# Kernel optimization log

Hardware: AMD Instinct MI355X
Metric: run time of the kernel (lower is better)

Reference implementation:

```python
import jax, jax.numpy as jnp
import numpy as np
from jax import lax

BN_EPS = 1e-3
SLOPE = 0.1
CLUSTER_TEMP = 30.0
K = 16
FEAT = 4096  # 8*8*64


def conv_bn_lrelu(x, w, b, g, beta, m, v):
    # Conv2d stride 2, padding 1 (NCHW / OIHW), then eval-mode BatchNorm, then LeakyReLU.
    y = lax.conv_general_dilated(x, w, window_strides=(2, 2), padding=((1, 1), (1, 1)),
                                 dimension_numbers=("NCHW", "OIHW", "NCHW"))
    y = y + b[None, :, None, None]
    scale = g / jnp.sqrt(v + BN_EPS)
    y = y * scale[None, :, None, None] + (beta - m * scale)[None, :, None, None]
    return jnp.where(y > 0, y, SLOPE * y)


def soft_kmeans(data, mu, num_iter, ct):
    # Row L2-normalize (equivalent to diag(1/||x||) @ data)
    data = data / jnp.linalg.norm(data, axis=1, keepdims=True)
    for _ in range(num_iter):
        dist = data @ mu.T                      # [N, K]
        r = jax.nn.softmax(ct * dist, axis=1)   # [N, K]
        mu = (r.T @ data) / r.sum(axis=0)[:, None]  # [K, F]
    dist = data @ mu.T
    r = jax.nn.softmax(ct * dist, axis=1)
    return mu, r, dist


def setup_inputs() -> dict:
    key = jax.random.key(0)
    ks = jax.random.split(key, 12)
    d = {}
    d["x"] = jax.random.normal(ks[0], (256, 3, 64, 64), dtype=jnp.float32)
    # conv1: 3 -> 128
    d["conv1_w"] = jax.random.normal(ks[1], (128, 3, 3, 3), dtype=jnp.float32) * 0.05
    d["conv1_b"] = jnp.zeros((128,), jnp.float32)
    d["bn1_g"] = jnp.ones((128,), jnp.float32)
    d["bn1_b"] = jnp.zeros((128,), jnp.float32)
    d["bn1_m"] = jax.random.normal(ks[2], (128,), dtype=jnp.float32) * 0.1
    d["bn1_v"] = jax.random.uniform(ks[3], (128,), minval=0.5, maxval=1.5, dtype=jnp.float32)
    # conv2: 128 -> 256
    d["conv2_w"] = jax.random.normal(ks[4], (256, 128, 3, 3), dtype=jnp.float32) * 0.02
    d["conv2_b"] = jnp.zeros((256,), jnp.float32)
    d["bn2_g"] = jnp.ones((256,), jnp.float32)
    d["bn2_b"] = jnp.zeros((256,), jnp.float32)
    d["bn2_m"] = jax.random.normal(ks[5], (256,), dtype=jnp.float32) * 0.1
    d["bn2_v"] = jax.random.uniform(ks[6], (256,), minval=0.5, maxval=1.5, dtype=jnp.float32)
    # conv3: 256 -> 64
    d["conv3_w"] = jax.random.normal(ks[7], (64, 256, 3, 3), dtype=jnp.float32) * 0.02
    d["conv3_b"] = jnp.zeros((64,), jnp.float32)
    d["bn3_g"] = jnp.ones((64,), jnp.float32)
    d["bn3_b"] = jnp.zeros((64,), jnp.float32)
    d["bn3_m"] = jax.random.normal(ks[8], (64,), dtype=jnp.float32) * 0.1
    d["bn3_v"] = jax.random.uniform(ks[9], (64,), minval=0.5, maxval=1.5, dtype=jnp.float32)
    # initial cluster centers, torch.rand(K, F)
    d["mu0"] = jax.random.uniform(ks[10], (K, FEAT), dtype=jnp.float32)
    d["num_iter"] = 10
    return d


def reference(x, conv1_w, conv1_b, bn1_g, bn1_b, bn1_m, bn1_v,
              conv2_w, conv2_b, bn2_g, bn2_b, bn2_m, bn2_v,
              conv3_w, conv3_b, bn3_g, bn3_b, bn3_m, bn3_v,
              mu0, num_iter):
    h = conv_bn_lrelu(x, conv1_w, conv1_b, bn1_g, bn1_b, bn1_m, bn1_v)   # [B,128,32,32]
    h = conv_bn_lrelu(h, conv2_w, conv2_b, bn2_g, bn2_b, bn2_m, bn2_v)   # [B,256,16,16]
    h = conv_bn_lrelu(h, conv3_w, conv3_b, bn3_g, bn3_b, bn3_m, bn3_v)   # [B,64,8,8]
    embeds = h.reshape(-1, FEAT)                                          # [B, 4096]
    mu_init, _, _ = soft_kmeans(embeds, mu0, num_iter, CLUSTER_TEMP)
    _, r, _ = soft_kmeans(embeds, lax.stop_gradient(mu_init), 1, CLUSTER_TEMP)
    return r
```

## Files before the change

kernel.cpp:

```cpp
#include <hip/hip_runtime.h>
#include <stdint.h>
#include <stddef.h>

typedef unsigned short u16;
typedef __attribute__((ext_vector_type(8))) short short8;
typedef __attribute__((ext_vector_type(4))) float f32x4;
typedef __attribute__((ext_vector_type(4))) int int4v;

__device__ __forceinline__ float bf2f(u16 u) {
    unsigned x = ((unsigned)u) << 16;
    return __uint_as_float(x);
}
__device__ __forceinline__ u16 f2bf(float f) {
    unsigned x = __float_as_uint(f);
    unsigned r = (x + 0x7fffu + ((x >> 16) & 1u)) >> 16;
    return (u16)r;
}
__device__ __forceinline__ float ldin(const void* p, size_t i, int isbf) {
    return isbf ? bf2f(((const u16*)p)[i]) : ((const float*)p)[i];
}
__device__ __forceinline__ int detect_bf(const void* v1) {
    const u16* ub = (const u16*)v1;
    int ok = 1;
#pragma unroll
    for (int i = 0; i < 16; i++) {
        float f = bf2f(ub[i]);
        if (!(f >= 0.4f && f <= 1.6f)) ok = 0;
    }
    return ok;
}
__device__ __forceinline__ int sw(int r, int c8) {
    return r * 32 + (((c8) ^ (r & 3)) << 3);
}

struct PrepArgs {
    const void *w1, *w2, *w3;
    u16 *W1p, *W2p, *W3p;
    const void *b1, *g1, *be1, *m1, *v1;
    const void *b2, *g2, *be2, *m2, *v2;
    const void *b3, *g3, *be3, *m3, *v3;
    float *es1, *esh1, *es2, *esh2, *es3, *esh3;
    u16 *zb;
};
__device__ __forceinline__ void packw_body(const void* src, u16* dst, int CI, int Kp,
                                           int total, int blk, int t, int isbf) {
    int p = blk * 256 + t;
    if (p >= total) return;
    int co = p / Kp, k = p - co * Kp;
    int tap = k / CI, ci = k - tap * CI;
    u16 v = 0;
    if (tap < 9) {
        size_t si = (size_t)(co * CI + ci) * 9 + tap;
        v = isbf ? ((const u16*)src)[si] : f2bf(((const float*)src)[si]);
    }
    dst[p] = v;
}
__global__ __launch_bounds__(256) void kprep_all(PrepArgs A) {
    int b = blockIdx.x, t = threadIdx.x;
    int isbf = detect_bf(A.v1);
    if (b < 1152) {
        packw_body(A.w2, A.W2p, 128, 1152, 256 * 1152, b, t, isbf);
    } else if (b < 1728) {
        packw_body(A.w3, A.W3p, 256, 2304, 64 * 2304, b - 1152, t, isbf);
    } else if (b < 1744) {
        packw_body(A.w1, A.W1p, 3, 32, 128 * 32, b - 1728, t, isbf);
    } else {
        if (b == 1745) A.zb[t] = 0;
        int u = (b - 1744) * 256 + t;
        const void *bb, *g, *be, *m, *v;
        float *es, *esh;
        int c;
        if (u < 128)      { c = u;       bb=A.b1; g=A.g1; be=A.be1; m=A.m1; v=A.v1; es=A.es1; esh=A.esh1; }
        else if (u < 384) { c = u - 128; bb=A.b2; g=A.g2; be=A.be2; m=A.m2; v=A.v2; es=A.es2; esh=A.esh2; }
        else if (u < 448) { c = u - 384; bb=A.b3; g=A.g3; be=A.be3; m=A.m3; v=A.v3; es=A.es3; esh=A.esh3; }
        else return;
        float sc = ldin(g, c, isbf) / sqrtf(ldin(v, c, isbf) + 1e-3f);
        float sh = (ldin(bb, c, isbf) - ldin(m, c, isbf)) * sc + ldin(be, c, isbf);
        es[c] = sc;
        esh[c] = sh;
    }
}

__global__ void kfallback(u16* __restrict__ out) {
    int i = blockIdx.x * 256 + threadIdx.x;
    if (i < 4096) out[i] = f2bf(0.0625f);
}

__global__ __launch_bounds__(256) void im2col1(const void* __restrict__ x,
                                               u16* __restrict__ A1,
                                               const void* __restrict__ v1ref) {
    int n = blockIdx.x, t = threadIdx.x;
    int isbf = detect_bf(v1ref);
    __shared__ u16 xs[3 * 64 * 64];
    if (isbf) {
        const u16* xp = (const u16*)x + (size_t)n * 12288;
#pragma unroll
        for (int i = t * 8; i < 12288; i += 2048)
            *(int4v*)&xs[i] = *(const int4v*)&xp[i];
    } else {
        const float* xp = (const float*)x + (size_t)n * 12288;
#pragma unroll
        for (int i = t * 4; i < 12288; i += 1024) {
            float4 v = *(const float4*)&xp[i];
            xs[i] = f2bf(v.x); xs[i + 1] = f2bf(v.y);
            xs[i + 2] = f2bf(v.z); xs[i + 3] = f2bf(v.w);
        }
    }
    __syncthreads();
#pragma unroll
    for (int rr = 0; rr < 4; rr++) {
        int m = rr * 256 + t;
        int ox = m & 31, oy = m >> 5;
        alignas(16) u16 row[32];
#pragma unroll
        for (int k = 0; k < 32; k++) {
            u16 val = 0;
            if (k < 27) {
                int tap = k / 3, ci = k - 3 * tap;
                int ky = tap / 3, kx = tap - 3 * ky;
                int iy = 2 * oy - 1 + ky, ix = 2 * ox - 1 + kx;
                if ((unsigned)iy < 64u && (unsigned)ix < 64u)
                    val = xs[ci * 4096 + iy * 64 + ix];
            }
            row[k] = val;
        }
        int4v* dst = (int4v*)(A1 + ((size_t)n * 1024 + m) * 32);
        const int4v* srcv = (const int4v*)row;
#pragma unroll
        for (int q = 0; q < 4; q++) dst[q] = srcv[q];
    }
}

__global__ __launch_bounds__(256) void gemm_conv1(
    const u16* __restrict__ A1, const u16* __restrict__ W,
    const float* __restrict__ es, const float* __restrict__ esh,
    u16* __restrict__ OutB) {
    alignas(16) __shared__ u16 As[128 * 32];
    alignas(16) __shared__ u16 Bs[128 * 32];
    const int t = threadIdx.x;
    const int m0 = blockIdx.x * 128;
    const int lane = t & 63, w = t >> 6;
    const int wm = w & 1, wn = w >> 1;
    const int rA = t >> 2, c8 = t & 3, koff = c8 * 8;

#pragma unroll
    for (int j = 0; j < 2; j++) {
        int4v va = *(const int4v*)(A1 + (size_t)(m0 + j * 64 + rA) * 32 + koff);
        *(int4v*)&As[sw(j * 64 + rA, c8)] = va;
        int4v vb = *(const int4v*)(W + (size_t)(j * 64 + rA) * 32 + koff);
        *(int4v*)&Bs[sw(j * 64 + rA, c8)] = vb;
    }
    __syncthreads();
    const int qc = lane >> 4, fr = lane & 15;
    short8 af[4], bf[4];
#pragma unroll
    for (int i = 0; i < 4; i++) af[i] = *(const short8*)&As[sw(wm * 64 + i * 16 + fr, qc)];
#pragma unroll
    for (int j = 0; j < 4; j++) bf[j] = *(const short8*)&Bs[sw(wn * 64 + j * 16 + fr, qc)];
    f32x4 acc[4][4];
#pragma unroll
    for (int i = 0; i < 4; i++)
#pragma unroll
        for (int j = 0; j < 4; j++) {
#pragma unroll
            for (int q = 0; q < 4; q++) acc[i][j][q] = 0.f;
            acc[i][j] = __builtin_amdgcn_mfma_f32_16x16x32_bf16(af[i], bf[j], acc[i][j], 0, 0, 0);
        }
    float scv[4], shv[4];
#pragma unroll
    for (int j = 0; j < 4; j++) {
        int c = wn * 64 + j * 16 + fr;
        scv[j] = es[c];
        shv[j] = esh[c];
    }
#pragma unroll
    for (int i = 0; i < 4; i++) {
#pragma unroll
        for (int rg = 0; rg < 4; rg++) {
            int m = m0 + wm * 64 + i * 16 + qc * 4 + rg;
            int ox = m & 31, oy = (m >> 5) & 31, n = m >> 10;
            u16* orow = OutB + ((size_t)(n * 32 + oy) * 32 + ox) * 128 + wn * 64 + fr;
#pragma unroll
            for (int j = 0; j < 4; j++) {
                float v = acc[i][j][rg] * scv[j] + shv[j];
                v = (v > 0.f) ? v : 0.1f * v;
                orow[j * 16] = f2bf(v);
            }
        }
    }
}

__global__ __launch_bounds__(512, 2) void gemm_conv2(
    const u16* __restrict__ h1, const u16* __restrict__ W,
    const float* __restrict__ es, const float* __restrict__ esh,
    u16* __restrict__ OutB, const u16* __restrict__ zb) {
    alignas(16) __shared__ u16 smem[4 * 16384];
    u16* const Ab0 = smem;
    u16* const Ab1 = smem + 16384;
    u16* const Bb0 = smem + 32768;
    u16* const Bb1 = smem + 49152;

    const int t = threadIdx.x;
    const int w = t >> 6, l = t & 63;
    const int img = blockIdx.x;
    const int wm = w >> 2, wn = w & 3;
    const int fr = l & 15, qc = l >> 4;

    int aiy0[4], aix0[4], ac8e[4];
    int brow[4];
#pragma unroll
    for (int i = 0; i < 4; ++i) {
        int gi = w * 256 + i * 64 + l;
        int r = gi >> 3, c8d = gi & 7;
        int c8s = c8d ^ (r & 7);
        int oy = r >> 4, ox = r & 15;
        aiy0[i] = 2 * oy - 1;
        aix0[i] = 2 * ox - 1;
        ac8e[i] = c8s * 8;
        brow[i] = r * 1152 + c8s * 8;
    }
    auto mkA = [&](int i, int ky, int kx) -> const u16* {
        int iy = aiy0[i] + ky, ix = aix0[i] + kx;
        if ((unsigned)iy < 32u && (unsigned)ix < 32u)
            return h1 + (size_t)(((img * 32 + iy) * 32 + ix) * 128 + ac8e[i]);
        return zb;
    };
    auto stage = [&](const u16* src, u16* ldsbase, int i) {
        __builtin_amdgcn_global_load_lds(
            (const __attribute__((address_space(1))) void*)src,
            (__attribute__((address_space(3))) void*)(ldsbase + (w * 4 + i) * 512),
            16, 0, 0);
    };

    f32x4 acc[8][4];
#pragma unroll
    for (int mi = 0; mi < 8; ++mi)
#pragma unroll
        for (int nj = 0; nj < 4; ++nj)
#pragma unroll
            for (int q = 0; q < 4; ++q) acc[mi][nj][q] = 0.0f;

    auto do_tile = [&](const u16* A, const u16* B) {
#pragma unroll
        for (int kk = 0; kk < 2; ++kk) {
            const int c8 = kk * 4 + qc;
            short8 a[8], b[4];
#pragma unroll
            for (int q = 0; q < 8; ++q) {
                int row = wm * 128 + q * 16 + fr;
                a[q] = *(const short8*)(A + row * 64 + ((c8 ^ (row & 7)) << 3));
            }
#pragma unroll
            for (int j = 0; j < 4; ++j) {
                int row = wn * 64 + j * 16 + fr;
                b[j] = *(const short8*)(B + row * 64 + ((c8 ^ (row & 7)) << 3));
            }
            __builtin_amdgcn_s_setprio(1);
#pragma unroll
            for (int q = 0; q < 8; ++q)
#pragma unroll
                for (int j = 0; j < 4; ++j)
                    acc[q][j] = __builtin_amdgcn_mfma_f32_16x16x32_bf16(
                        a[q], b[j], acc[q][j], 0, 0, 0);
            __builtin_amdgcn_s_setprio(0);
        }
    };

    const u16* pcur[4];
#pragma unroll
    for (int i = 0; i < 4; ++i) pcur[i] = mkA(i, 0, 0);
#pragma unroll
    for (int i = 0; i < 4; ++i) {
        stage(pcur[i], Ab0, i);
        stage(W + brow[i], Bb0, i);
    }
#pragma unroll
    for (int i = 0; i < 4; ++i) {
        stage(pcur[i] + 64, Ab1, i);
        stage(W + brow[i] + 64, Bb1, i);
    }

    for (int tap = 0; tap < 9; ++tap) {
        asm volatile("s_waitcnt vmcnt(8)" ::: "memory");
        __builtin_amdgcn_s_barrier();
        do_tile(Ab0, Bb0);
        asm volatile("s_waitcnt lgkmcnt(0)" ::: "memory");
        __builtin_amdgcn_s_barrier();
        if (tap < 8) {
            const int tap2 = tap + 1;
            const int ky2 = (tap2 >= 6) ? 2 : (tap2 >= 3) ? 1 : 0;
            const int kx2 = tap2 - 3 * ky2;
#pragma unroll
            for (int i = 0; i < 4; ++i) pcur[i] = mkA(i, ky2, kx2);
#pragma unroll
            for (int i = 0; i < 4; ++i) {
                stage(pcur[i], Ab0, i);
                stage(W + brow[i] + (2 * tap + 2) * 64, Bb0, i);
            }
        }
        if (tap < 8) {
            asm volatile("s_waitcnt vmcnt(8)" ::: "memory");
        } else {
            asm volatile("s_waitcnt vmcnt(0)" ::: "memory");
        }
        __builtin_amdgcn_s_barrier();
        do_tile(Ab1, Bb1);
        asm volatile("s_waitcnt lgkmcnt(0)" ::: "memory");
        __builtin_amdgcn_s_barrier();
        if (tap < 8) {
#pragma unroll
            for (int i = 0; i < 4; ++i) {
                stage(pcur[i] + 64, Ab1, i);
                stage(W + brow[i] + (2 * tap + 3) * 64, Bb1, i);
            }
        }
    }

    float scv[4], shv[4];
#pragma unroll
    for (int nj = 0; nj < 4; ++nj) {
        int c = wn * 64 + nj * 16 + fr;
        scv[nj] = es[c];
        shv[nj] = esh[c];
    }
#pragma unroll
    for (int mi = 0; mi < 8; ++mi) {
#pragma unroll
        for (int rg = 0; rg < 4; ++rg) {
            int r = wm * 128 + mi * 16 + qc * 4 + rg;
            u16* orow = OutB + ((size_t)img * 256 + r) * 256 + wn * 64 + fr;
#pragma unroll
            for (int nj = 0; nj < 4; ++nj) {
                float v = acc[mi][nj][rg] * scv[nj] + shv[nj];
                v = (v > 0.f) ? v : 0.1f * v;
                orow[nj * 16] = f2bf(v);
            }
        }
    }
}

__global__ __launch_bounds__(256) void gemm_conv3f(
    const u16* __restrict__ Asrc, const u16* __restrict__ W,
    const float* __restrict__ es3, const float* __restrict__ esh3,
    float* __restrict__ dat, u16* __restrict__ datbf) {
    constexpr int CIN = 256, KTOT = 2304, IH = 16;
    constexpr int CC = 8, SM = 2, SN = 2;

    alignas(16) __shared__ u16 As[64 * 32];
    alignas(16) __shared__ u16 Bs[64 * 32];
    __shared__ float red[4];

    const int t = threadIdx.x;
    const int lid = blockIdx.x;
    const int xcd = lid & 7, slot = lid >> 3;
    const int img = xcd * 32 + slot;
    const int m0 = img * 64;
    const int lane = t & 63, w = t >> 6;
    const int wm = w & 1, wn = w >> 1;
    const int rA = t >> 2, c8 = t & 3, koff = c8 * 8;
    const int fr = lane & 15, qc = lane >> 4;

    f32x4 acc[SM][SN];
#pragma unroll
    for (int i = 0; i < SM; i++)
#pragma unroll
        for (int j = 0; j < SN; j++)
#pragma unroll
            for (int q = 0; q < 4; q++) acc[i][j][q] = 0.0f;

    const int aox = rA & 7, aoy = (rA >> 3) & 7;
    auto mkoffs = [&](int tap) -> int {
        int ky = tap / 3, kx = tap - 3 * ky;
        int iy = 2 * aoy - 1 + ky, ix = 2 * aox - 1 + kx;
        if ((unsigned)iy < (unsigned)IH && (unsigned)ix < (unsigned)IH)
            return ((img * IH + iy) * IH + ix) * CIN;
        return -0x40000000;
    };
    const u16* Wrow = W + (size_t)rA * KTOT + koff;

    int offs_cur = mkoffs(0), offs_nxt;
    const int4v zerov = (int4v){0, 0, 0, 0};
    int4v bufA[2], bufB[2];
#pragma unroll
    for (int pp = 0; pp < 2; pp++) {
        bufA[pp] = (offs_cur >= 0)
                       ? *(const int4v*)(Asrc + offs_cur + pp * 32 + koff)
                       : zerov;
        bufB[pp] = *(const int4v*)(Wrow + pp * 32);
    }

    int flat = 0;
    for (int tap = 0; tap < 9; tap++) {
        offs_nxt = (tap < 8) ? mkoffs(tap + 1) : -0x40000000;
#pragma unroll
        for (int cc = 0; cc < CC; cc++, flat++) {
            const int pb_ = flat & 1;
            *(int4v*)&As[sw(rA, c8)] = bufA[pb_];
            *(int4v*)&Bs[sw(rA, c8)] = bufB[pb_];
            __syncthreads();
            {
                const int cc2 = cc + 2;
                const bool intap = (cc2 < CC);
                const int cci = intap ? cc2 : cc2 - CC;
                int o = intap ? offs_cur : offs_nxt;
                bufA[pb_] = (o >= 0) ? *(const int4v*)(Asrc + o + cci * 32 + koff) : zerov;
                const bool wvalid = intap || (tap < 8);
                const int wk = (intap ? tap : tap + 1) * CIN + cci * 32;
                bufB[pb_] = wvalid ? *(const int4v*)(Wrow + wk) : zerov;
            }
            short8 af[SM], bf[SN];
#pragma unroll
            for (int i = 0; i < SM; i++)
                af[i] = *(const short8*)&As[sw(wm * 32 + i * 16 + fr, qc)];
#pragma unroll
            for (int j = 0; j < SN; j++)
                bf[j] = *(const short8*)&Bs[sw(wn * 32 + j * 16 + fr, qc)];
#pragma unroll
            for (int i = 0; i < SM; i++)
#pragma unroll
                for (int j = 0; j < SN; j++)
                    acc[i][j] = __builtin_amdgcn_mfma_f32_16x16x32_bf16(
                        af[i], bf[j], acc[i][j], 0, 0, 0);
            __syncthreads();
        }
        offs_cur = offs_nxt;
    }

    float vals[SM][SN][4];
    float ssq = 0.f;
#pragma unroll
    for (int j = 0; j < SN; j++) {
        int c = wn * 32 + j * 16 + fr;
        float sc = es3[c], sh = esh3[c];
#pragma unroll
        for (int i = 0; i < SM; i++) {
#pragma unroll
            for (int rg = 0; rg < 4; rg++) {
                float v = acc[i][j][rg] * sc + sh;
                v = (v > 0.f) ? v : 0.1f * v;
                vals[i][j][rg] = v;
                ssq += v * v;
            }
        }
    }
#pragma unroll
    for (int off = 32; off > 0; off >>= 1) ssq += __shfl_xor(ssq, off);
    if (lane == 0) red[w] = ssq;
    __syncthreads();
    float inv = 1.0f / sqrtf(red[0] + red[1] + red[2] + red[3]);
#pragma unroll
    for (int j = 0; j < SN; j++) {
        int c = wn * 32 + j * 16 + fr;
#pragma unroll
        for (int i = 0; i < SM; i++) {
#pragma unroll
            for (int rg = 0; rg < 4; rg++) {
                int row = wm * 32 + i * 16 + qc * 4 + rg;
                size_t idx = (size_t)img * 4096 + c * 64 + row;
                float v = vals[i][j][rg] * inv;
                dat[idx] = v;
                datbf[idx] = f2bf(v);
            }
        }
    }
}

__global__ __launch_bounds__(256) void kgr(const u16* __restrict__ dbf,
                                           const float* __restrict__ dat,
                                           const void* __restrict__ mu0,
                                           float* __restrict__ Gp,
                                           float* __restrict__ rb0,
                                           const void* __restrict__ v1ref) {
    const int b = blockIdx.x, t = threadIdx.x;
    __shared__ float part[16][4];
    __shared__ float ds[16];

    if (b < 64) {
        const int tile = b & 15, s = b >> 4;
        const int m0 = (tile & 3) * 64, n0 = (tile >> 2) * 64;
        const int lane = t & 63, w = t >> 6;
        const int wm = w & 1, wn = w >> 1;
        const int fr = lane & 15, qc = lane >> 4;

        f32x4 acc[2][2];
#pragma unroll
        for (int i = 0; i < 2; i++)
#pragma unroll
            for (int j = 0; j < 2; j++)
#pragma unroll
                for (int q = 0; q < 4; q++) acc[i][j][q] = 0.0f;

        const u16* a0p = dbf + (size_t)(m0 + wm * 32 + fr) * 4096 + s * 1024 + qc * 8;
        const u16* a1p = a0p + 16 * 4096;
        const u16* b0p = dbf + (size_t)(n0 + wn * 32 + fr) * 4096 + s * 1024 + qc * 8;
        const u16* b1p = b0p + 16 * 4096;

        short8 Pa0[4], Pa1[4], Pb0[4], Pb1[4];
        short8 Qa0[4], Qa1[4], Qb0[4], Qb1[4];
        auto ldc = [&](short8* A0, short8* A1, short8* B0, short8* B1, int c) {
#pragma unroll
            for (int u = 0; u < 4; ++u) {
                const int o = c * 128 + u * 32;
                A0[u] = *(const short8*)(a0p + o);
                A1[u] = *(const short8*)(a1p + o);
                B0[u] = *(const short8*)(b0p + o);
                B1[u] = *(const short8*)(b1p + o);
            }
        };
        auto mmc = [&](short8* A0, short8* A1, short8* B0, short8* B1) {
#pragma unroll
            for (int u = 0; u < 4; ++u) {
                acc[0][0] = __builtin_amdgcn_mfma_f32_16x16x32_bf16(A0[u], B0[u], acc[0][0], 0, 0, 0);
                acc[0][1] = __builtin_amdgcn_mfma_f32_16x16x32_bf16(A0[u], B1[u], acc[0][1], 0, 0, 0);
                acc[1][0] = __builtin_amdgcn_mfma_f32_16x16x32_bf16(A1[u], B0[u], acc[1][0], 0, 0, 0);
                acc[1][1] = __builtin_amdgcn_mfma_f32_16x16x32_bf16(A1[u], B1[u], acc[1][1], 0, 0, 0);
            }
        };
        ldc(Pa0, Pa1, Pb0, Pb1, 0);
#pragma unroll
        for (int c = 0; c < 4; ++c) {
            ldc(Qa0, Qa1, Qb0, Qb1, 2 * c + 1);
            mmc(Pa0, Pa1, Pb0, Pb1);
            if (c < 3) ldc(Pa0, Pa1, Pb0, Pb1, 2 * c + 2);
            mmc(Qa0, Qa1, Qb0, Qb1);
        }

        float* gp = Gp + (size_t)s * 65536;
#pragma unroll
        for (int j = 0; j < 2; j++) {
            int cc = n0 + wn * 32 + j * 16 + fr;
#pragma unroll
            for (int i = 0; i < 2; i++)
#pragma unroll
                for (int rg = 0; rg < 4; rg++) {
                    int row = m0 + wm * 32 + i * 16 + qc * 4 + rg;
                    gp[row * 256 + cc] = acc[i][j][rg];
                }
        }
    } else {
        const int n = b - 64;
        const int isbf = detect_bf(v1ref);
        const int lane = t & 63, wv = t >> 6;
        float d[16];
#pragma unroll
        for (int j = 0; j < 16; j++) d[j] = dat[(size_t)n * 4096 + j * 256 + t];
#pragma unroll
        for (int k = 0; k < 16; k++) {
            float a = 0.f;
            if (isbf) {
                const u16* mp = (const u16*)mu0 + (size_t)k * 4096;
#pragma unroll
                for (int j = 0; j < 16; j++) a = fmaf(d[j], bf2f(mp[j * 256 + t]), a);
            } else {
                const float* mp = (const float*)mu0 + (size_t)k * 4096;
#pragma unroll
                for (int j = 0; j < 16; j++) a = fmaf(d[j], mp[j * 256 + t], a);
            }
#pragma unroll
            for (int off = 32; off > 0; off >>= 1) a += __shfl_xor(a, off);
            if (lane == 0) part[k][wv] = a;
        }
        __syncthreads();
        if (t < 16) {
            float dk = part[t][0] + part[t][1] + part[t][2] + part[t][3];
            ds[t] = dk;
            __syncthreads();
            float mx = -1e30f;
#pragma unroll
            for (int j = 0; j < 16; j++) mx = fmaxf(mx, ds[j]);
            float sum = 0.f;
#pragma unroll
            for (int j = 0; j < 16; j++) sum += __expf(30.f * (ds[j] - mx));
            rb0[n * 16 + t] = __expf(30.f * (dk - mx)) / sum;
        }
    }
}

__global__ __launch_bounds__(256) void kcomb(const float* __restrict__ Gp,
                                             u16* __restrict__ Ghi,
                                             u16* __restrict__ Glo) {
    const int i = (blockIdx.x * 256 + threadIdx.x) * 4;
    f32x4 s0 = *(const f32x4*)(Gp + i);
    f32x4 s1 = *(const f32x4*)(Gp + 65536 + i);
    f32x4 s2 = *(const f32x4*)(Gp + 131072 + i);
    f32x4 s3 = *(const f32x4*)(Gp + 196608 + i);
    unsigned long long ph = 0, pl = 0;
#pragma unroll
    for (int q = 0; q < 4; q++) {
        float v = ((s0[q] + s1[q]) + s2[q]) + s3[q];
        u16 hi = f2bf(v);
        u16 lo = f2bf(v - bf2f(hi));
        ph |= ((unsigned long long)hi) << (16 * q);
        pl |= ((unsigned long long)lo) << (16 * q);
    }
    *(unsigned long long*)(Ghi + i) = ph;
    *(unsigned long long*)(Glo + i) = pl;
}

__global__ __launch_bounds__(1024) void kmiter(const u16* __restrict__ Ghi,
                                               const u16* __restrict__ Glo,
                                               const float* __restrict__ rb0,
                                               void* __restrict__ dout,
                                               const void* __restrict__ v1ref) {
    const int t = threadIdx.x;
    const int isbf = detect_bf(v1ref);
    const int lane = t & 63, w = t >> 6;
    const int i0 = w * 16;
    const int col = lane & 15;
    const int q = lane >> 4;

    __shared__ u16 rThi[2][16 * 264];
    __shared__ u16 rTlo[2][16 * 264];
    __shared__ float part[2][16][17];

    const u16* Ahirow = Ghi + (size_t)(i0 + col) * 256 + q * 8;
    const u16* Alorow = Glo + (size_t)(i0 + col) * 256 + q * 8;

    {
        float rv[4];
#pragma unroll
        for (int rg = 0; rg < 4; rg++) {
            int row = i0 + q * 4 + rg;
            float v = rb0[row * 16 + col];
            rv[rg] = v;
            u16 hi = f2bf(v);
            rThi[0][col * 264 + row] = hi;
            rTlo[0][col * 264 + row] = f2bf(v - bf2f(hi));
        }
        float s0 = rv[0] + rv[1] + rv[2] + rv[3];
        s0 += __shfl_xor(s0, 16);
        s0 += __shfl_xor(s0, 32);
        if (lane < 16) part[0][w][lane] = s0;
    }
    __syncthreads();
    float rsc = 0.f;
#pragma unroll
    for (int ww = 0; ww < 16; ww++) rsc += part[0][ww][col];

    int cur = 0;
    for (int iter = 0; iter < 11; iter++) {
        f32x4 acc0 = {0.f, 0.f, 0.f, 0.f};
        f32x4 acc1 = {0.f, 0.f, 0.f, 0.f};
#pragma unroll
        for (int s = 0; s < 4; s++) {
            {
                short8 ah = *(const short8*)(Ahirow + s * 32);
                short8 al = *(const short8*)(Alorow + s * 32);
                short8 bh = *(const short8*)&rThi[cur][col * 264 + s * 32 + q * 8];
                short8 bl = *(const short8*)&rTlo[cur][col * 264 + s * 32 + q * 8];
                acc0 = __builtin_amdgcn_mfma_f32_16x16x32_bf16(ah, bh, acc0, 0, 0, 0);
                acc0 = __builtin_amdgcn_mfma_f32_16x16x32_bf16(al, bh, acc0, 0, 0, 0);
                acc0 = __builtin_amdgcn_mfma_f32_16x16x32_bf16(ah, bl, acc0, 0, 0, 0);
            }
            {
                short8 ah = *(const short8*)(Ahirow + (s + 4) * 32);
                short8 al = *(const short8*)(Alorow + (s + 4) * 32);
                short8 bh = *(const short8*)&rThi[cur][col * 264 + (s + 4) * 32 + q * 8];
                short8 bl = *(const short8*)&rTlo[cur][col * 264 + (s + 4) * 32 + q * 8];
                acc1 = __builtin_amdgcn_mfma_f32_16x16x32_bf16(ah, bh, acc1, 0, 0, 0);
                acc1 = __builtin_amdgcn_mfma_f32_16x16x32_bf16(al, bh, acc1, 0, 0, 0);
                acc1 = __builtin_amdgcn_mfma_f32_16x16x32_bf16(ah, bl, acc1, 0, 0, 0);
            }
        }
        float nv[4];
#pragma unroll
        for (int rg = 0; rg < 4; rg++) {
            float dk = (acc0[rg] + acc1[rg]) / rsc;
            float mx = dk;
#pragma unroll
            for (int o = 1; o < 16; o <<= 1) mx = fmaxf(mx, __shfl_xor(mx, o));
            float e = __expf(30.f * (dk - mx));
            float ssum = e;
#pragma unroll
            for (int o = 1; o < 16; o <<= 1) ssum += __shfl_xor(ssum, o);
            nv[rg] = e / ssum;
        }
        if (iter < 10) {
            const int nxt = cur ^ 1;
#pragma unroll
            for (int rg = 0; rg < 4; rg++) {
                int row = i0 + q * 4 + rg;
                u16 hi = f2bf(nv[rg]);
                rThi[nxt][col * 264 + row] = hi;
                rTlo[nxt][col * 264 + row] = f2bf(nv[rg] - bf2f(hi));
            }
            float s0 = nv[0] + nv[1] + nv[2] + nv[3];
            s0 += __shfl_xor(s0, 16);
            s0 += __shfl_xor(s0, 32);
            if (lane < 16) part[nxt][w][lane] = s0;
            __syncthreads();
            rsc = 0.f;
#pragma unroll
            for (int ww = 0; ww < 16; ww++) rsc += part[nxt][ww][col];
            cur = nxt;
        } else {
#pragma unroll
            for (int rg = 0; rg < 4; rg++) {
                int row = i0 + q * 4 + rg;
                if (isbf) ((u16*)dout)[row * 16 + col] = f2bf(nv[rg]);
                else ((float*)dout)[row * 16 + col] = nv[rg];
            }
        }
    }
}

extern "C" void kernel_launch(void* const* d_in, const int* in_sizes, int n_in,
                              void* d_out, int out_size, void* d_ws, size_t ws_size,
                              hipStream_t stream) {
    const void* x   = d_in[0];
    const void* w1  = d_in[1];
    const void* b1  = d_in[2];
    const void* g1  = d_in[3];
    const void* be1 = d_in[4];
    const void* m1  = d_in[5];
    const void* v1  = d_in[6];
    const void* w2  = d_in[7];
    const void* b2  = d_in[8];
    const void* g2  = d_in[9];
    const void* be2 = d_in[10];
    const void* m2  = d_in[11];
    const void* v2  = d_in[12];
    const void* w3  = d_in[13];
    const void* b3  = d_in[14];
    const void* g3  = d_in[15];
    const void* be3 = d_in[16];
    const void* m3  = d_in[17];
    const void* v3  = d_in[18];
    const void* mu0 = d_in[19];

    char* p = (char*)d_ws;
    size_t used = 0;
    auto alloc = [&](size_t bytes) -> char* {
        char* q = p;
        size_t rb = (bytes + 255) & ~(size_t)255;
        p += rb;
        used += rb;
        return q;
    };
    float* rb0 = (float*)alloc(4096 * 4);
    u16* Ghi = (u16*)alloc((size_t)65536 * 2);
    u16* Glo = (u16*)alloc((size_t)65536 * 2);
    float* Gp = (float*)alloc((size_t)4 * 65536 * 4);
    u16* W1p = (u16*)alloc((size_t)128 * 32 * 2);
    u16* W2p = (u16*)alloc((size_t)256 * 1152 * 2);
    u16* W3p = (u16*)alloc((size_t)64 * 2304 * 2);
    float* es1 = (float*)alloc(128 * 4);
    float* esh1 = (float*)alloc(128 * 4);
    float* es2 = (float*)alloc(256 * 4);
    float* esh2 = (float*)alloc(256 * 4);
    float* es3 = (float*)alloc(64 * 4);
    float* esh3 = (float*)alloc(64 * 4);
    u16* zb = (u16*)alloc(512);
    const size_t R1 = (size_t)256 * 32 * 32 * 128 * 2;
    const size_t R2 = (size_t)256 * 16 * 16 * 256 * 2;
    char* reg1 = alloc(R1);
    char* reg2 = alloc(R2);
    u16* h1 = (u16*)reg1;
    u16* A1 = (u16*)reg2;
    u16* h2 = (u16*)reg2;
    float* dat = (float*)reg1;
    u16* datbf = (u16*)(reg1 + 4194304);

    if (used > ws_size) {
        kfallback<<<16, 256, 0, stream>>>((u16*)d_out);
        return;
    }

    PrepArgs pa = {w1, w2, w3, W1p, W2p, W3p,
                   b1, g1, be1, m1, v1, b2, g2, be2, m2, v2, b3, g3, be3, m3, v3,
                   es1, esh1, es2, esh2, es3, esh3, zb};
    kprep_all<<<1746, 256, 0, stream>>>(pa);
    im2col1<<<256, 256, 0, stream>>>(x, A1, v1);
    gemm_conv1<<<dim3(2048), 256, 0, stream>>>(A1, W1p, es1, esh1, h1);
    gemm_conv2<<<dim3(256), 512, 0, stream>>>(h1, W2p, es2, esh2, h2, zb);
    gemm_conv3f<<<dim3(256), 256, 0, stream>>>(h2, W3p, es3, esh3, dat, datbf);
    kgr<<<dim3(320), 256, 0, stream>>>(datbf, dat, mu0, Gp, rb0, v1);
    kcomb<<<dim3(64), 256, 0, stream>>>(Gp, Ghi, Glo);
    kmiter<<<1, 1024, 0, stream>>>(Ghi, Glo, rb0, d_out, v1);
}
```

Baseline: 268.5 us.

## Use direct global-to-LDS loads with wider K tiles in conv3 GEMM

```diff
diff --git a/kernel.cpp b/kernel.cpp
--- a/kernel.cpp
+++ b/kernel.cpp
@@ -274,18 +274,16 @@
         stage(pcur[i], Ab0, i);
         stage(W + brow[i], Bb0, i);
     }
-#pragma unroll
-    for (int i = 0; i < 4; ++i) {
-        stage(pcur[i] + 64, Ab1, i);
-        stage(W + brow[i] + 64, Bb1, i);
-    }
 
     for (int tap = 0; tap < 9; ++tap) {
-        asm volatile("s_waitcnt vmcnt(8)" ::: "memory");
-        __builtin_amdgcn_s_barrier();
+        __syncthreads();
+#pragma unroll
+        for (int i = 0; i < 4; ++i) {
+            stage(pcur[i] + 64, Ab1, i);
+            stage(W + brow[i] + (2 * tap + 1) * 64, Bb1, i);
+        }
         do_tile(Ab0, Bb0);
-        asm volatile("s_waitcnt lgkmcnt(0)" ::: "memory");
-        __builtin_amdgcn_s_barrier();
+        __syncthreads();
         if (tap < 8) {
             const int tap2 = tap + 1;
             const int ky2 = (tap2 >= 6) ? 2 : (tap2 >= 3) ? 1 : 0;
@@ -298,22 +296,7 @@
                 stage(W + brow[i] + (2 * tap + 2) * 64, Bb0, i);
             }
         }
-        if (tap < 8) {
-            asm volatile("s_waitcnt vmcnt(8)" ::: "memory");
-        } else {
-            asm volatile("s_waitcnt vmcnt(0)" ::: "memory");
-        }
-        __builtin_amdgcn_s_barrier();
         do_tile(Ab1, Bb1);
-        asm volatile("s_waitcnt lgkmcnt(0)" ::: "memory");
-        __builtin_amdgcn_s_barrier();
-        if (tap < 8) {
-#pragma unroll
-            for (int i = 0; i < 4; ++i) {
-                stage(pcur[i] + 64, Ab1, i);
-                stage(W + brow[i] + (2 * tap + 3) * 64, Bb1, i);
-            }
-        }
     }
 
     float scv[4], shv[4];
@@ -342,98 +325,122 @@
 __global__ __launch_bounds__(256) void gemm_conv3f(
     const u16* __restrict__ Asrc, const u16* __restrict__ W,
     const float* __restrict__ es3, const float* __restrict__ esh3,
-    float* __restrict__ dat, u16* __restrict__ datbf) {
-    constexpr int CIN = 256, KTOT = 2304, IH = 16;
-    constexpr int CC = 8, SM = 2, SN = 2;
-
-    alignas(16) __shared__ u16 As[64 * 32];
-    alignas(16) __shared__ u16 Bs[64 * 32];
+    float* __restrict__ dat, u16* __restrict__ datbf,
+    const u16* __restrict__ zb) {
+    alignas(16) __shared__ u16 smem[4 * 4096];
     __shared__ float red[4];
+    u16* const AbP[2] = {smem, smem + 4096};
+    u16* const BbP[2] = {smem + 8192, smem + 12288};
 
     const int t = threadIdx.x;
+    const int w = t >> 6, l = t & 63;
     const int lid = blockIdx.x;
     const int xcd = lid & 7, slot = lid >> 3;
     const int img = xcd * 32 + slot;
-    const int m0 = img * 64;
-    const int lane = t & 63, w = t >> 6;
     const int wm = w & 1, wn = w >> 1;
-    const int rA = t >> 2, c8 = t & 3, koff = c8 * 8;
-    const int fr = lane & 15, qc = lane >> 4;
-
-    f32x4 acc[SM][SN];
-#pragma unroll
-    for (int i = 0; i < SM; i++)
-#pragma unroll
-        for (int j = 0; j < SN; j++)
+    const int fr = l & 15, qc = l >> 4;
+
+    int aiy0[2], aix0[2], ac8e[2];
+    int brow[2];
+#pragma unroll
+    for (int i = 0; i < 2; ++i) {
+        int g = w * 128 + i * 64 + l;
+        int r = g >> 3, c8d = g & 7;
+        int c8s = c8d ^ (r & 7);
+        int oy = r >> 3, ox = r & 7;
+        aiy0[i] = 2 * oy - 1;
+        aix0[i] = 2 * ox - 1;
+        ac8e[i] = c8s * 8;
+        brow[i] = r * 2304 + c8s * 8;
+    }
+    auto mkA = [&](int i, int ky, int kx) -> const u16* {
+        int iy = aiy0[i] + ky, ix = aix0[i] + kx;
+        if ((unsigned)iy < 16u && (unsigned)ix < 16u)
+            return Asrc + (size_t)(((img * 16 + iy) * 16 + ix) * 256 + ac8e[i]);
+        return zb;
+    };
+    auto stage = [&](const u16* src, u16* ldsbase, int i) {
+        __builtin_amdgcn_global_load_lds(
+            (const __attribute__((address_space(1))) void*)src,
+            (__attribute__((address_space(3))) void*)(ldsbase + (w * 2 + i) * 512),
+            16, 0, 0);
+    };
+
+    f32x4 acc[2][2];
+#pragma unroll
+    for (int i = 0; i < 2; i++)
+#pragma unroll
+        for (int j = 0; j < 2; j++)
 #pragma unroll
             for (int q = 0; q < 4; q++) acc[i][j][q] = 0.0f;
 
-    const int aox = rA & 7, aoy = (rA >> 3) & 7;
-    auto mkoffs = [&](int tap) -> int {
-        int ky = tap / 3, kx = tap - 3 * ky;
-        int iy = 2 * aoy - 1 + ky, ix = 2 * aox - 1 + kx;
-        if ((unsigned)iy < (unsigned)IH && (unsigned)ix < (unsigned)IH)
-            return ((img * IH + iy) * IH + ix) * CIN;
-        return -0x40000000;
+    auto do_tile = [&](const u16* A, const u16* B) {
+#pragma unroll
+        for (int kk = 0; kk < 2; ++kk) {
+            const int c8 = kk * 4 + qc;
+            short8 a[2], b[2];
+#pragma unroll
+            for (int i = 0; i < 2; ++i) {
+                int row = wm * 32 + i * 16 + fr;
+                a[i] = *(const short8*)(A + row * 64 + ((c8 ^ (row & 7)) << 3));
+            }
+#pragma unroll
+            for (int j = 0; j < 2; ++j) {
+                int row = wn * 32 + j * 16 + fr;
+                b[j] = *(const short8*)(B + row * 64 + ((c8 ^ (row & 7)) << 3));
+            }
+            __builtin_amdgcn_s_setprio(1);
+#pragma unroll
+            for (int i = 0; i < 2; ++i)
+#pragma unroll
+                for (int j = 0; j < 2; ++j)
+                    acc[i][j] = __builtin_amdgcn_mfma_f32_16x16x32_bf16(
+                        a[i], b[j], acc[i][j], 0, 0, 0);
+            __builtin_amdgcn_s_setprio(0);
+        }
     };
-    const u16* Wrow = W + (size_t)rA * KTOT + koff;
-
-    int offs_cur = mkoffs(0), offs_nxt;
-    const int4v zerov = (int4v){0, 0, 0, 0};
-    int4v bufA[2], bufB[2];
-#pragma unroll
-    for (int pp = 0; pp < 2; pp++) {
-        bufA[pp] = (offs_cur >= 0)
-                       ? *(const int4v*)(Asrc + offs_cur + pp * 32 + koff)
-                       : zerov;
-        bufB[pp] = *(const int4v*)(Wrow + pp * 32);
+
+    const u16* pcur[2];
+#pragma unroll
+    for (int i = 0; i < 2; ++i) pcur[i] = mkA(i, 0, 0);
+#pragma unroll
+    for (int i = 0; i < 2; ++i) {
+        stage(pcur[i], AbP[0], i);
+        stage(W + brow[i], BbP[0], i);
     }
 
     int flat = 0;
-    for (int tap = 0; tap < 9; tap++) {
-        offs_nxt = (tap < 8) ? mkoffs(tap + 1) : -0x40000000;
-#pragma unroll
-        for (int cc = 0; cc < CC; cc++, flat++) {
-            const int pb_ = flat & 1;
-            *(int4v*)&As[sw(rA, c8)] = bufA[pb_];
-            *(int4v*)&Bs[sw(rA, c8)] = bufB[pb_];
+    for (int tap = 0; tap < 9; ++tap) {
+        for (int q4 = 0; q4 < 4; ++q4, ++flat) {
+            const int cb = flat & 1;
             __syncthreads();
-            {
-                const int cc2 = cc + 2;
-                const bool intap = (cc2 < CC);
-                const int cci = intap ? cc2 : cc2 - CC;
-                int o = intap ? offs_cur : offs_nxt;
-                bufA[pb_] = (o >= 0) ? *(const int4v*)(Asrc + o + cci * 32 + koff) : zerov;
-                const bool wvalid = intap || (tap < 8);
-                const int wk = (intap ? tap : tap + 1) * CIN + cci * 32;
-                bufB[pb_] = wvalid ? *(const int4v*)(Wrow + wk) : zerov;
-            }
-            short8 af[SM], bf[SN];
-#pragma unroll
-            for (int i = 0; i < SM; i++)
-                af[i] = *(const short8*)&As[sw(wm * 32 + i * 16 + fr, qc)];
-#pragma unroll
-            for (int j = 0; j < SN; j++)
-                bf[j] = *(const short8*)&Bs[sw(wn * 32 + j * 16 + fr, qc)];
-#pragma unroll
-            for (int i = 0; i < SM; i++)
-#pragma unroll
-                for (int j = 0; j < SN; j++)
-                    acc[i][j] = __builtin_amdgcn_mfma_f32_16x16x32_bf16(
-                        af[i], bf[j], acc[i][j], 0, 0, 0);
-            __syncthreads();
-        }
-        offs_cur = offs_nxt;
-    }
-
-    float vals[SM][SN][4];
+            int ntap = tap, nq = q4 + 1;
+            if (nq == 4) { nq = 0; ntap = tap + 1; }
+            if (ntap < 9) {
+                if (nq == 0) {
+                    const int ky = (ntap >= 6) ? 2 : (ntap >= 3) ? 1 : 0;
+                    const int kx = ntap - 3 * ky;
+#pragma unroll
+                    for (int i = 0; i < 2; ++i) pcur[i] = mkA(i, ky, kx);
+                }
+#pragma unroll
+                for (int i = 0; i < 2; ++i) {
+                    stage(pcur[i] + nq * 64, AbP[cb ^ 1], i);
+                    stage(W + brow[i] + ntap * 256 + nq * 64, BbP[cb ^ 1], i);
+                }
+            }
+            do_tile(AbP[cb], BbP[cb]);
+        }
+    }
+
+    float vals[2][2][4];
     float ssq = 0.f;
 #pragma unroll
-    for (int j = 0; j < SN; j++) {
+    for (int j = 0; j < 2; j++) {
         int c = wn * 32 + j * 16 + fr;
         float sc = es3[c], sh = esh3[c];
 #pragma unroll
-        for (int i = 0; i < SM; i++) {
+        for (int i = 0; i < 2; i++) {
 #pragma unroll
             for (int rg = 0; rg < 4; rg++) {
                 float v = acc[i][j][rg] * sc + sh;
@@ -445,14 +452,14 @@
     }
 #pragma unroll
     for (int off = 32; off > 0; off >>= 1) ssq += __shfl_xor(ssq, off);
-    if (lane == 0) red[w] = ssq;
+    if (l == 0) red[w] = ssq;
     __syncthreads();
     float inv = 1.0f / sqrtf(red[0] + red[1] + red[2] + red[3]);
 #pragma unroll
-    for (int j = 0; j < SN; j++) {
+    for (int j = 0; j < 2; j++) {
         int c = wn * 32 + j * 16 + fr;
 #pragma unroll
-        for (int i = 0; i < SM; i++) {
+        for (int i = 0; i < 2; i++) {
 #pragma unroll
             for (int rg = 0; rg < 4; rg++) {
                 int row = wm * 32 + i * 16 + qc * 4 + rg;
@@ -773,7 +780,7 @@
     im2col1<<<256, 256, 0, stream>>>(x, A1, v1);
     gemm_conv1<<<dim3(2048), 256, 0, stream>>>(A1, W1p, es1, esh1, h1);
     gemm_conv2<<<dim3(256), 512, 0, stream>>>(h1, W2p, es2, esh2, h2, zb);
-    gemm_conv3f<<<dim3(256), 256, 0, stream>>>(h2, W3p, es3, esh3, dat, datbf);
+    gemm_conv3f<<<dim3(256), 256, 0, stream>>>(h2, W3p, es3, esh3, dat, datbf, zb);
     kgr<<<dim3(320), 256, 0, stream>>>(datbf, dat, mu0, Gp, rb0, v1);
     kcomb<<<dim3(64), 256, 0, stream>>>(Gp, Ghi, Glo);
     kmiter<<<1, 1024, 0, stream>>>(Ghi, Glo, rb0, d_out, v1);
```

Result: faster. 257.6 us (-4.1%).
